# Optimization experiments

Measured on AMD Instinct MI355X. Metric: run time of the kernel, lower is better.

Reference implementation:

```python
import jax, jax.numpy as jnp
import numpy as np

S, C, E, G, H = 8192, 21, 128, 36, 1024  # seq_len, context_len, embed_dim, gazet_dim, hidden_dim
V_IN = 8000
T = 32              # tagset size incl. BOS/EOS
START, STOP = 30, 31
NEG = -10000.0


def setup_inputs() -> dict:
    key = jax.random.key(0)
    ks = jax.random.split(key, 10)
    contexts = jax.random.randint(ks[0], (S, C), 0, V_IN)
    gazet = jax.random.uniform(ks[1], (S, C, G), dtype=jnp.float32)
    train_labels = jax.random.randint(ks[2], (S,), 0, 30)  # base tags only
    emb = jax.random.normal(ks[3], (V_IN, E), dtype=jnp.float32) * 0.1
    D = C * (E + G)
    w1 = jax.random.normal(ks[4], (H, D), dtype=jnp.float32) / np.sqrt(D)
    b1 = jnp.zeros((H,), dtype=jnp.float32)
    w2 = jax.random.normal(ks[5], (T, H), dtype=jnp.float32) / np.sqrt(H)
    b2 = jnp.zeros((T,), dtype=jnp.float32)
    trans = jax.random.normal(ks[6], (T, T), dtype=jnp.float32)
    trans = trans.at[START, :].set(NEG)   # nothing transitions into START... (row = next tag)
    trans = trans.at[:, STOP].set(NEG)    # nothing leaves STOP (col = prev tag)
    return {"contexts": contexts, "gazet": gazet, "train_labels": train_labels,
            "emb": emb, "w1": w1, "b1": b1, "w2": w2, "b2": b2, "trans": trans}


def _feats(contexts, gazet, emb, w1, b1, w2, b2):
    x = jnp.concatenate([emb[contexts], gazet], axis=2)      # [S, C, E+G]
    x = x.reshape(x.shape[0], -1)                            # [S, C*(E+G)]
    h = jax.nn.relu(x @ w1.T + b1)                           # [S, H]  (dropout = identity in eval)
    return h @ w2.T + b2                                     # [S, T]


def _crf_forward(feats, trans):
    alpha0 = jnp.full((T,), NEG, dtype=feats.dtype).at[START].set(0.0)

    def step(alpha, feat):
        # scores[next, prev] = alpha[prev] + trans[next, prev] + feat[next]
        scores = alpha[None, :] + trans + feat[:, None]
        return jax.nn.logsumexp(scores, axis=1), None

    alpha, _ = jax.lax.scan(step, alpha0, feats)
    return jax.nn.logsumexp(alpha + trans[STOP])


def _gold_score(feats, tags, trans):
    tags_ext = jnp.concatenate([jnp.array([START], dtype=tags.dtype), tags])
    trans_sc = jnp.sum(trans[tags_ext[1:], tags_ext[:-1]])
    emit_sc = jnp.sum(feats[jnp.arange(feats.shape[0]), tags])
    return trans_sc + emit_sc + trans[STOP, tags[-1]]


def reference(contexts, gazet, train_labels, emb, w1, b1, w2, b2, trans):
    feats = _feats(contexts, gazet, emb, w1, b1, w2, b2)
    fwd = _crf_forward(feats, trans)
    gold = _gold_score(feats, train_labels, trans)
    return fwd - gold  # neg_log_likelihood (scalar)
```

## Files before the change

### kernel.cpp

```cpp
#include <hip/hip_runtime.h>

#define S_LEN 8192
#define C_CTX 21
#define E_DIM 128
#define G_DIM 36
#define H_DIM 1024
#define T_TAG 32
#define D_RAW 3444
#define DP 3456
#define GZP 768
#define START_TAG 30
#define STOP_TAG 31
#define NEGV -10000.0f
#define K_CHUNKS 64
#define L_CHUNK 128

typedef __bf16 bf16_t;
typedef __bf16 bf16x4 __attribute__((ext_vector_type(4)));
typedef __bf16 bf16x8 __attribute__((ext_vector_type(8)));
typedef float  f32x4  __attribute__((ext_vector_type(4)));

__device__ inline void async_copy16(const bf16_t* g, bf16_t* l) {
    __builtin_amdgcn_global_load_lds(
        (const __attribute__((address_space(1))) void*)g,
        (__attribute__((address_space(3))) void*)l, 16, 0, 0);
}

__global__ void build_all(const int* __restrict__ ctx, const float* __restrict__ gz,
                          const float* __restrict__ emb, const float* __restrict__ w1,
                          bf16_t* __restrict__ Xg, bf16_t* __restrict__ W,
                          bf16_t* __restrict__ EB) {
    const int b = blockIdx.x;
    if (b < 1024) {
        const int h = b;
        for (int g = threadIdx.x; g < DP / 4; g += 256) {
            bf16x4 o;
            if (g < 672) {
                const int knew = g * 4;
                const float4 v = *(const float4*)&w1[(size_t)h * D_RAW + (knew >> 7) * 164 + (knew & 127)];
                o = bf16x4{(bf16_t)v.x, (bf16_t)v.y, (bf16_t)v.z, (bf16_t)v.w};
            } else {
                const int m = g * 4 - 2688;
                float t[4];
#pragma unroll
                for (int u = 0; u < 4; ++u) {
                    const int mm = m + u;
                    t[u] = (mm < 756) ? w1[(size_t)h * D_RAW + (mm / 36) * 164 + 128 + (mm % 36)] : 0.f;
                }
                o = bf16x4{(bf16_t)t[0], (bf16_t)t[1], (bf16_t)t[2], (bf16_t)t[3]};
            }
            *(bf16x4*)&W[(size_t)h * DP + g * 4] = o;
        }
    } else if (b < 3072) {
        const int s_base = (b - 1024) * 4;
        for (int g = threadIdx.x; g < 4 * 192; g += 256) {
            const int r = g / 192, gg = g - r * 192;
            const int s = s_base + r;
            bf16x4 o = bf16x4{(bf16_t)0.f, (bf16_t)0.f, (bf16_t)0.f, (bf16_t)0.f};
            if (gg < 189) {
                const float4 v = *(const float4*)&gz[(size_t)s * 756 + gg * 4];
                o = bf16x4{(bf16_t)v.x, (bf16_t)v.y, (bf16_t)v.z, (bf16_t)v.w};
            }
            *(bf16x4*)&Xg[(size_t)s * GZP + gg * 4] = o;
        }
    } else {
        const size_t base = (size_t)(b - 3072) * 2048;
        for (int g = threadIdx.x; g < 512; g += 256) {
            const float4 v = *(const float4*)&emb[base + g * 4];
            bf16x4 o = bf16x4{(bf16_t)v.x, (bf16_t)v.y, (bf16_t)v.z, (bf16_t)v.w};
            *(bf16x4*)&EB[base + g * 4] = o;
        }
    }
}

__global__ __launch_bounds__(512) void gemm1(const int* __restrict__ ctx,
                                             const bf16_t* __restrict__ EB,
                                             const bf16_t* __restrict__ Xg,
                                             const bf16_t* __restrict__ W,
                                             const float* __restrict__ b1,
                                             const float* __restrict__ w2,
                                             const float* __restrict__ b2,
                                             float* __restrict__ Fp) {
    __shared__ bf16_t As[3][256 * 64];
    __shared__ bf16_t Bs[3][128 * 64];
    __shared__ unsigned short ctxs[256 * 21];
    const int tid  = threadIdx.x;
    const int wave = tid >> 6, lane = tid & 63;
    const int s0 = blockIdx.x * 256, h0 = blockIdx.y * 128;
    const int wm = (wave >> 1) * 64;
    const int wn = (wave & 1) * 64;

    const int arow = tid >> 3;
    const int akg  = (tid & 7) ^ (arow & 7);
    const bf16_t* gB = W + (size_t)(h0 + arow) * DP + akg * 8;

    const int lrow  = lane & 15;
    const int khalf = lane >> 4;
    const int lr7   = lrow & 7;

#define STAGE_B(buf, k0, i) async_copy16(gB + (size_t)(i) * 64 * DP + (k0), &Bs[buf][((i) * 512 + tid) * 8])

    for (int j = tid; j < 256 * C_CTX; j += 512)
        ctxs[j] = (unsigned short)ctx[s0 * C_CTX + j];
    asm volatile("s_waitcnt lgkmcnt(0)" ::: "memory");
    __builtin_amdgcn_s_barrier();

    {
        const int cva = ctxs[(arow      ) * 21], cvb = ctxs[(arow +  64) * 21];
        const int cvc = ctxs[(arow + 128) * 21], cvd = ctxs[(arow + 192) * 21];
        const int ea0 = akg * 8;
        async_copy16(EB + (size_t)cva * 128 + ea0, &As[0][(0 * 512 + tid) * 8]);
        async_copy16(EB + (size_t)cvb * 128 + ea0, &As[0][(1 * 512 + tid) * 8]);
        async_copy16(EB + (size_t)cvc * 128 + ea0, &As[0][(2 * 512 + tid) * 8]);
        async_copy16(EB + (size_t)cvd * 128 + ea0, &As[0][(3 * 512 + tid) * 8]);
        STAGE_B(0, 0, 0); STAGE_B(0, 0, 1);
        const int ea1 = 64 + akg * 8;
        async_copy16(EB + (size_t)cva * 128 + ea1, &As[1][(0 * 512 + tid) * 8]);
        async_copy16(EB + (size_t)cvb * 128 + ea1, &As[1][(1 * 512 + tid) * 8]);
        async_copy16(EB + (size_t)cvc * 128 + ea1, &As[1][(2 * 512 + tid) * 8]);
        async_copy16(EB + (size_t)cvd * 128 + ea1, &As[1][(3 * 512 + tid) * 8]);
        STAGE_B(1, 64, 0); STAGE_B(1, 64, 1);
    }
    asm volatile("s_waitcnt vmcnt(6)" ::: "memory");
    __builtin_amdgcn_s_barrier();

    f32x4 acc[4][4] = {};
    const int NT = DP / 64;
    int rb = 0;
    for (int t = 0; t < NT; ++t) {
        const int  sb = (rb == 0) ? 2 : rb - 1;
        const int  tt = t + 2;
        const bool st = tt < NT;
        const bool semb = st && (tt < 42);

        int cv0 = 0, cv1 = 0, cv2 = 0, cv3 = 0;
        if (semb) {
            const int c_ = tt >> 1;
            cv0 = ctxs[(arow      ) * 21 + c_];
            cv1 = ctxs[(arow +  64) * 21 + c_];
            cv2 = ctxs[(arow + 128) * 21 + c_];
            cv3 = ctxs[(arow + 192) * 21 + c_];
        }

        bf16x8 a[2][2][2];
        bf16x8 b[2][2][2];
#pragma unroll
        for (int ks = 0; ks < 2; ++ks) {
            const int kgr = ((ks * 4 + khalf) ^ lr7) * 8;
#pragma unroll
            for (int sp = 0; sp < 2; ++sp)
#pragma unroll
                for (int mt = 0; mt < 2; ++mt)
                    a[sp][ks][mt] = *(const bf16x8*)&As[rb][(wm + sp * 32 + mt * 16 + lrow) * 64 + kgr];
#pragma unroll
            for (int qn = 0; qn < 2; ++qn)
#pragma unroll
                for (int nt = 0; nt < 2; ++nt)
                    b[qn][ks][nt] = *(const bf16x8*)&Bs[rb][(wn + qn * 32 + nt * 16 + lrow) * 64 + kgr];
        }
        if (st) {
            if (semb) {
                const int e0 = (tt & 1) * 64 + akg * 8;
                async_copy16(EB + (size_t)cv0 * 128 + e0, &As[sb][(0 * 512 + tid) * 8]);
                async_copy16(EB + (size_t)cv1 * 128 + e0, &As[sb][(1 * 512 + tid) * 8]);
                async_copy16(EB + (size_t)cv2 * 128 + e0, &As[sb][(2 * 512 + tid) * 8]);
                async_copy16(EB + (size_t)cv3 * 128 + e0, &As[sb][(3 * 512 + tid) * 8]);
            } else {
                const int m0 = (tt - 42) * 64 + akg * 8;
#pragma unroll
                for (int i = 0; i < 4; ++i)
                    async_copy16(Xg + (size_t)(s0 + arow + i * 64) * GZP + m0, &As[sb][(i * 512 + tid) * 8]);
            }
            STAGE_B(sb, tt * 64, 0); STAGE_B(sb, tt * 64, 1);
        }
        __builtin_amdgcn_s_barrier();
        __builtin_amdgcn_s_setprio(1);
#pragma unroll
        for (int ks = 0; ks < 2; ++ks)
#pragma unroll
            for (int sp = 0; sp < 2; ++sp)
#pragma unroll
                for (int qn = 0; qn < 2; ++qn)
#pragma unroll
                    for (int mt = 0; mt < 2; ++mt)
#pragma unroll
                        for (int nt = 0; nt < 2; ++nt)
                            acc[sp * 2 + mt][qn * 2 + nt] = __builtin_amdgcn_mfma_f32_16x16x32_bf16(
                                a[sp][ks][mt], b[qn][ks][nt], acc[sp * 2 + mt][qn * 2 + nt], 0, 0, 0);
        __builtin_amdgcn_s_setprio(0);
        if (st)              asm volatile("s_waitcnt vmcnt(6)" ::: "memory");
        else if (t + 1 < NT) asm volatile("s_waitcnt vmcnt(0)" ::: "memory");
        __builtin_amdgcn_s_barrier();
        rb = (rb == 2) ? 0 : rb + 1;
    }
#undef STAGE_B

    bf16_t* Hl = &As[0][0];
    bf16_t* Wl = &Bs[0][0];

    {
        const int t8 = tid >> 4;
        const int hl = tid & 15;
        const float* wsrc = w2 + (size_t)t8 * H_DIM + h0 + hl * 8;
        const float4 y0 = *(const float4*)wsrc;
        const float4 y1 = *(const float4*)(wsrc + 4);
        bf16x8 wv = {(bf16_t)y0.x, (bf16_t)y0.y, (bf16_t)y0.z, (bf16_t)y0.w,
                     (bf16_t)y1.x, (bf16_t)y1.y, (bf16_t)y1.z, (bf16_t)y1.w};
        *(bf16x8*)&Wl[(t8 * 16 + (hl ^ (t8 & 7))) * 8] = wv;
    }

    const int crow = (lane >> 4) * 4;
    const int ccol = lane & 15;
#pragma unroll
    for (int nt = 0; nt < 4; ++nt) {
        const int jl = wn + nt * 16 + ccol;
        const float bv = b1[h0 + jl];
#pragma unroll
        for (int mt = 0; mt < 4; ++mt) {
#pragma unroll
            for (int r = 0; r < 4; ++r) {
                const int sl = wm + mt * 16 + crow + r;
                const float v = acc[mt][nt][r] + bv;
                Hl[sl * 128 + ((jl >> 3) ^ (sl & 7)) * 8 + (jl & 7)] = (bf16_t)fmaxf(v, 0.f);
            }
        }
    }
    __syncthreads();

    f32x4 acc2[2][2] = {};
    const int wm2 = wave * 32;
#pragma unroll
    for (int ks = 0; ks < 4; ++ks) {
        const int slot = ((ks * 4 + khalf) ^ lr7) * 8;
        bf16x8 ah[2], bw[2];
#pragma unroll
        for (int mt = 0; mt < 2; ++mt)
            ah[mt] = *(const bf16x8*)&Hl[(wm2 + mt * 16 + lrow) * 128 + slot];
#pragma unroll
        for (int nt = 0; nt < 2; ++nt)
            bw[nt] = *(const bf16x8*)&Wl[(nt * 16 + lrow) * 128 + slot];
#pragma unroll
        for (int mt = 0; mt < 2; ++mt)
#pragma unroll
            for (int nt = 0; nt < 2; ++nt)
                acc2[mt][nt] = __builtin_amdgcn_mfma_f32_16x16x32_bf16(ah[mt], bw[nt], acc2[mt][nt], 0, 0, 0);
    }
    const int bj = h0 >> 7;
#pragma unroll
    for (int nt = 0; nt < 2; ++nt) {
        const int tcol = nt * 16 + ccol;
        const float badd = (bj == 7) ? b2[tcol] : 0.f;
#pragma unroll
        for (int mt = 0; mt < 2; ++mt) {
#pragma unroll
            for (int r = 0; r < 4; ++r) {
                const int sr = s0 + wm2 + mt * 16 + crow + r;
                Fp[((size_t)bj * S_LEN + sr) * T_TAG + tcol] = acc2[mt][nt][r] + badd;
            }
        }
    }
}

__global__ __launch_bounds__(512) void crfA(const float* __restrict__ Fp,
                                            const float* __restrict__ trans,
                                            float* __restrict__ QT,
                                            float* __restrict__ sigma,
                                            float* __restrict__ Fsum) {
    __shared__ float fl[L_CHUNK * 32];
    __shared__ float vb[8][64];
    const int c    = blockIdx.x >> 2;
    const int tid  = threadIdx.x;
    const int wave = tid >> 6;
    const int lane = tid & 63;
    const int n    = lane & 31;
    const int h    = lane >> 5;
    const int p    = ((blockIdx.x & 3) << 3) + wave;
    const int s0   = c * L_CHUNK;
    for (int i = tid; i < L_CHUNK * 32; i += 512) {
        const size_t idx = (size_t)s0 * 32 + i;
        float accf = 0.f;
#pragma unroll
        for (int j = 0; j < 8; ++j) accf += Fp[(size_t)j * S_LEN * T_TAG + idx];
        fl[i] = accf;
        Fsum[idx] = accf;
    }
    __syncthreads();

    float etl[16];
#pragma unroll
    for (int j = 0; j < 16; ++j) etl[j] = __expf(trans[n * 32 + h * 16 + j]);

    float* vrow = &vb[wave][0];
    float v  = __expf(trans[n * 32 + p] + fl[n]);
    float sg = 0.f;
    for (int s = 1; s < L_CHUNK; ++s) {
        vrow[lane] = v;
        __builtin_amdgcn_s_waitcnt(0xC07F);
        float a0 = 0.f, a1 = 0.f, a2 = 0.f, a3 = 0.f;
#pragma unroll
        for (int q = 0; q < 4; ++q) {
            const float4 wv = *(const float4*)&vrow[h * 16 + q * 4];
            a0 = __builtin_fmaf(etl[q * 4 + 0], wv.x, a0);
            a1 = __builtin_fmaf(etl[q * 4 + 1], wv.y, a1);
            a2 = __builtin_fmaf(etl[q * 4 + 2], wv.z, a2);
            a3 = __builtin_fmaf(etl[q * 4 + 3], wv.w, a3);
        }
        float part = (a0 + a1) + (a2 + a3);
        part += __shfl_xor(part, 32);
        v = __expf(fl[s * 32 + n]) * part;
        if ((s & 7) == 7) {
            float m = v;
#pragma unroll
            for (int off = 16; off; off >>= 1) m = fmaxf(m, __shfl_xor(m, off, 32));
            if (m > 0.f) { v *= 1.0f / m; sg += __logf(m); }
        }
    }
    if (h == 0) {
        QT[(c * 32 + p) * 32 + n] = v;
        if (n == 0) sigma[c * 32 + p] = sg;
    }
}

__global__ __launch_bounds__(1024) void crf_fold(const float* __restrict__ Qin,
                                                 const float* __restrict__ Sin,
                                                 const int fold, const int final,
                                                 float* __restrict__ Qout,
                                                 float* __restrict__ Sout,
                                                 const float* __restrict__ trans,
                                                 const float* __restrict__ F,
                                                 const int* __restrict__ lab,
                                                 float* __restrict__ out) {
    __shared__ float A[32][33];
    __shared__ float M[32][33];
    __shared__ float sgf[32];
    __shared__ float gred[16];
    __shared__ float gold_s;

    const int t = threadIdx.x;
    const int p = t >> 5, n = t & 31;
    const int c0 = blockIdx.x * fold;

    if (final) {
        float ga = 0.f;
        for (int s = t; s < S_LEN; s += 1024) {
            const int tg = lab[s];
            ga += F[(size_t)s * T_TAG + tg];
            const int tp = (s == 0) ? START_TAG : lab[s - 1];
            ga += trans[tg * T_TAG + tp];
        }
        if (t == 0) ga += trans[STOP_TAG * T_TAG + lab[S_LEN - 1]];
#pragma unroll
        for (int off = 32; off; off >>= 1) ga += __shfl_down(ga, off, 64);
        if ((t & 63) == 0) gred[t >> 6] = ga;
    }

    A[n][p] = Qin[(size_t)(c0 * 32 + p) * 32 + n];
    float sA = Sin[c0 * 32 + p];
    float mreg = Qin[(size_t)((c0 + 1) * 32 + p) * 32 + n];

    for (int i = 1; i < fold; ++i) {
        const float sMn = Sin[(c0 + i) * 32 + n];
        float mmax = sMn;
#pragma unroll
        for (int off = 16; off; off >>= 1) mmax = fmaxf(mmax, __shfl_xor(mmax, off, 32));
        const float sMp = Sin[(c0 + i) * 32 + p];
        __syncthreads();
        M[n][p] = mreg * __expf(sMp - mmax);
        if (i + 1 < fold) mreg = Qin[(size_t)((c0 + i + 1) * 32 + p) * 32 + n];
        __syncthreads();
        float acc = 0.f;
#pragma unroll 8
        for (int k = 0; k < 32; ++k)
            acc += M[n][k] * A[k][p];
        float cm = acc;
#pragma unroll
        for (int off = 16; off; off >>= 1) cm = fmaxf(cm, __shfl_xor(cm, off, 32));
        cm = fmaxf(cm, 1e-37f);
        __syncthreads();
        A[n][p] = acc / cm;
        sA = sA + mmax + __logf(cm);
    }
    __syncthreads();

    if (!final) {
        Qout[(size_t)(blockIdx.x * 32 + p) * 32 + n] = A[n][p];
        if (n == 0) Sout[blockIdx.x * 32 + p] = sA;
        return;
    }

    if (n == 0) sgf[p] = sA;
    if (t == 0) {
        float s = 0.f;
#pragma unroll
        for (int i = 0; i < 16; ++i) s += gred[i];
        gold_s = s;
    }
    __syncthreads();
    if (t < 32) {
        float v = A[t][START_TAG] * __expf(trans[STOP_TAG * T_TAG + t]);
#pragma unroll
        for (int off = 16; off; off >>= 1) v += __shfl_xor(v, off, 32);
        if (t == 0) out[0] = sgf[START_TAG] + __logf(v) - gold_s;
    }
}

extern "C" void kernel_launch(void* const* d_in, const int* in_sizes, int n_in,
                              void* d_out, int out_size, void* d_ws, size_t ws_size,
                              hipStream_t stream) {
    const int*   ctx   = (const int*)d_in[0];
    const float* gz    = (const float*)d_in[1];
    const int*   lab   = (const int*)d_in[2];
    const float* emb   = (const float*)d_in[3];
    const float* w1    = (const float*)d_in[4];
    const float* b1    = (const float*)d_in[5];
    const float* w2    = (const float*)d_in[6];
    const float* b2    = (const float*)d_in[7];
    const float* trans = (const float*)d_in[8];
    float* out = (float*)d_out;

    char* ws = (char*)d_ws;
    bf16_t* W1b = (bf16_t*)(ws + 0);
    bf16_t* EB  = (bf16_t*)(ws + 7077888);
    bf16_t* Xg  = (bf16_t*)(ws + 9126400);
    float*  Fp  = (float*)(ws + 21709312);
    float*  F   = (float*)(ws + 30097920);
    float*  QT  = (float*)(ws + 31146496);
    float*  sg  = (float*)(ws + 31408640);
    float*  Q1  = (float*)(ws + 31416832);
    float*  S1  = (float*)(ws + 31449600);

    build_all<<<3572, 256, 0, stream>>>(ctx, gz, emb, w1, Xg, W1b, EB);
    gemm1<<<dim3(S_LEN / 256, H_DIM / 128), 512, 0, stream>>>(ctx, EB, Xg, W1b, b1, w2, b2, Fp);
    crfA<<<K_CHUNKS * 4, 512, 0, stream>>>(Fp, trans, QT, sg, F);
    crf_fold<<<8, 1024, 0, stream>>>(QT, sg, 8, 0, Q1, S1, trans, F, lab, out);
    crf_fold<<<1, 1024, 0, stream>>>(Q1, S1, 8, 1, nullptr, nullptr, trans, F, lab, out);
}
```

Baseline: 240.9 us.

## Shrink GEMM1 tile to 128x128 with 256 threads and double buffering

The fused GEMM1 kernel moves from 256x128 tiles with 512 threads and a 3-stage async pipeline to 128x128 tiles with 256 threads and a 2-stage buffer. Each iteration now waits for all outstanding loads (vmcnt(0)) before the barrier. This cuts LDS use per block and doubles the grid, aiming for more resident blocks and better CU coverage. In exchange, each loaded W1 tile is reused across fewer rows, global traffic rises, and less load latency is hidden behind compute. The epilogue loop for w2 staging is adjusted to fit the smaller thread count.

```diff
diff --git a/kernel.cpp b/kernel.cpp
--- a/kernel.cpp
+++ b/kernel.cpp
@@ -73,7 +73,7 @@
     }
 }
 
-__global__ __launch_bounds__(512) void gemm1(const int* __restrict__ ctx,
+__global__ __launch_bounds__(256) void gemm1(const int* __restrict__ ctx,
                                              const bf16_t* __restrict__ EB,
                                              const bf16_t* __restrict__ Xg,
                                              const bf16_t* __restrict__ W,
@@ -81,12 +81,12 @@
                                              const float* __restrict__ w2,
                                              const float* __restrict__ b2,
                                              float* __restrict__ Fp) {
-    __shared__ bf16_t As[3][256 * 64];
-    __shared__ bf16_t Bs[3][128 * 64];
-    __shared__ unsigned short ctxs[256 * 21];
+    __shared__ bf16_t As[2][128 * 64];
+    __shared__ bf16_t Bs[2][128 * 64];
+    __shared__ unsigned short ctxs[128 * 21];
     const int tid  = threadIdx.x;
     const int wave = tid >> 6, lane = tid & 63;
-    const int s0 = blockIdx.x * 256, h0 = blockIdx.y * 128;
+    const int s0 = blockIdx.x * 128, h0 = blockIdx.y * 128;
     const int wm = (wave >> 1) * 64;
     const int wn = (wave & 1) * 64;
 
@@ -98,49 +98,31 @@
     const int khalf = lane >> 4;
     const int lr7   = lrow & 7;
 
-#define STAGE_B(buf, k0, i) async_copy16(gB + (size_t)(i) * 64 * DP + (k0), &Bs[buf][((i) * 512 + tid) * 8])
-
-    for (int j = tid; j < 256 * C_CTX; j += 512)
+    for (int j = tid; j < 128 * C_CTX; j += 256)
         ctxs[j] = (unsigned short)ctx[s0 * C_CTX + j];
     asm volatile("s_waitcnt lgkmcnt(0)" ::: "memory");
     __builtin_amdgcn_s_barrier();
 
     {
-        const int cva = ctxs[(arow      ) * 21], cvb = ctxs[(arow +  64) * 21];
-        const int cvc = ctxs[(arow + 128) * 21], cvd = ctxs[(arow + 192) * 21];
-        const int ea0 = akg * 8;
-        async_copy16(EB + (size_t)cva * 128 + ea0, &As[0][(0 * 512 + tid) * 8]);
-        async_copy16(EB + (size_t)cvb * 128 + ea0, &As[0][(1 * 512 + tid) * 8]);
-        async_copy16(EB + (size_t)cvc * 128 + ea0, &As[0][(2 * 512 + tid) * 8]);
-        async_copy16(EB + (size_t)cvd * 128 + ea0, &As[0][(3 * 512 + tid) * 8]);
-        STAGE_B(0, 0, 0); STAGE_B(0, 0, 1);
-        const int ea1 = 64 + akg * 8;
-        async_copy16(EB + (size_t)cva * 128 + ea1, &As[1][(0 * 512 + tid) * 8]);
-        async_copy16(EB + (size_t)cvb * 128 + ea1, &As[1][(1 * 512 + tid) * 8]);
-        async_copy16(EB + (size_t)cvc * 128 + ea1, &As[1][(2 * 512 + tid) * 8]);
-        async_copy16(EB + (size_t)cvd * 128 + ea1, &As[1][(3 * 512 + tid) * 8]);
-        STAGE_B(1, 64, 0); STAGE_B(1, 64, 1);
-    }
-    asm volatile("s_waitcnt vmcnt(6)" ::: "memory");
+        const int e0 = akg * 8;
+#pragma unroll
+        for (int i = 0; i < 4; ++i) {
+            const int cv = ctxs[(i * 32 + arow) * 21];
+            async_copy16(EB + (size_t)cv * 128 + e0, &As[0][(i * 256 + tid) * 8]);
+        }
+#pragma unroll
+        for (int i = 0; i < 4; ++i)
+            async_copy16(gB + (size_t)i * 32 * DP, &Bs[0][(i * 256 + tid) * 8]);
+    }
+    asm volatile("s_waitcnt vmcnt(0)" ::: "memory");
     __builtin_amdgcn_s_barrier();
 
     f32x4 acc[4][4] = {};
     const int NT = DP / 64;
-    int rb = 0;
     for (int t = 0; t < NT; ++t) {
-        const int  sb = (rb == 0) ? 2 : rb - 1;
-        const int  tt = t + 2;
+        const int cur = t & 1, nxt = cur ^ 1;
+        const int tt = t + 1;
         const bool st = tt < NT;
-        const bool semb = st && (tt < 42);
-
-        int cv0 = 0, cv1 = 0, cv2 = 0, cv3 = 0;
-        if (semb) {
-            const int c_ = tt >> 1;
-            cv0 = ctxs[(arow      ) * 21 + c_];
-            cv1 = ctxs[(arow +  64) * 21 + c_];
-            cv2 = ctxs[(arow + 128) * 21 + c_];
-            cv3 = ctxs[(arow + 192) * 21 + c_];
-        }
 
         bf16x8 a[2][2][2];
         bf16x8 b[2][2][2];
@@ -151,29 +133,32 @@
             for (int sp = 0; sp < 2; ++sp)
 #pragma unroll
                 for (int mt = 0; mt < 2; ++mt)
-                    a[sp][ks][mt] = *(const bf16x8*)&As[rb][(wm + sp * 32 + mt * 16 + lrow) * 64 + kgr];
+                    a[sp][ks][mt] = *(const bf16x8*)&As[cur][(wm + sp * 32 + mt * 16 + lrow) * 64 + kgr];
 #pragma unroll
             for (int qn = 0; qn < 2; ++qn)
 #pragma unroll
                 for (int nt = 0; nt < 2; ++nt)
-                    b[qn][ks][nt] = *(const bf16x8*)&Bs[rb][(wn + qn * 32 + nt * 16 + lrow) * 64 + kgr];
+                    b[qn][ks][nt] = *(const bf16x8*)&Bs[cur][(wn + qn * 32 + nt * 16 + lrow) * 64 + kgr];
         }
         if (st) {
-            if (semb) {
+            if (tt < 42) {
+                const int c_ = tt >> 1;
                 const int e0 = (tt & 1) * 64 + akg * 8;
-                async_copy16(EB + (size_t)cv0 * 128 + e0, &As[sb][(0 * 512 + tid) * 8]);
-                async_copy16(EB + (size_t)cv1 * 128 + e0, &As[sb][(1 * 512 + tid) * 8]);
-                async_copy16(EB + (size_t)cv2 * 128 + e0, &As[sb][(2 * 512 + tid) * 8]);
-                async_copy16(EB + (size_t)cv3 * 128 + e0, &As[sb][(3 * 512 + tid) * 8]);
+#pragma unroll
+                for (int i = 0; i < 4; ++i) {
+                    const int cv = ctxs[(i * 32 + arow) * 21 + c_];
+                    async_copy16(EB + (size_t)cv * 128 + e0, &As[nxt][(i * 256 + tid) * 8]);
+                }
             } else {
                 const int m0 = (tt - 42) * 64 + akg * 8;
 #pragma unroll
                 for (int i = 0; i < 4; ++i)
-                    async_copy16(Xg + (size_t)(s0 + arow + i * 64) * GZP + m0, &As[sb][(i * 512 + tid) * 8]);
+                    async_copy16(Xg + (size_t)(s0 + i * 32 + arow) * GZP + m0, &As[nxt][(i * 256 + tid) * 8]);
             }
-            STAGE_B(sb, tt * 64, 0); STAGE_B(sb, tt * 64, 1);
-        }
-        __builtin_amdgcn_s_barrier();
+#pragma unroll
+            for (int i = 0; i < 4; ++i)
+                async_copy16(gB + (size_t)i * 32 * DP + tt * 64, &Bs[nxt][(i * 256 + tid) * 8]);
+        }
         __builtin_amdgcn_s_setprio(1);
 #pragma unroll
         for (int ks = 0; ks < 2; ++ks)
@@ -188,19 +173,17 @@
                             acc[sp * 2 + mt][qn * 2 + nt] = __builtin_amdgcn_mfma_f32_16x16x32_bf16(
                                 a[sp][ks][mt], b[qn][ks][nt], acc[sp * 2 + mt][qn * 2 + nt], 0, 0, 0);
         __builtin_amdgcn_s_setprio(0);
-        if (st)              asm volatile("s_waitcnt vmcnt(6)" ::: "memory");
-        else if (t + 1 < NT) asm volatile("s_waitcnt vmcnt(0)" ::: "memory");
+        if (st) asm volatile("s_waitcnt vmcnt(0)" ::: "memory");
         __builtin_amdgcn_s_barrier();
-        rb = (rb == 2) ? 0 : rb + 1;
-    }
-#undef STAGE_B
+    }
 
     bf16_t* Hl = &As[0][0];
     bf16_t* Wl = &Bs[0][0];
 
-    {
-        const int t8 = tid >> 4;
-        const int hl = tid & 15;
+#pragma unroll
+    for (int rep = 0; rep < 2; ++rep) {
+        const int t8 = tid >> 3;
+        const int hl = (tid & 7) * 2 + rep;
         const float* wsrc = w2 + (size_t)t8 * H_DIM + h0 + hl * 8;
         const float4 y0 = *(const float4*)wsrc;
         const float4 y1 = *(const float4*)(wsrc + 4);
@@ -430,7 +413,7 @@
     float*  S1  = (float*)(ws + 31449600);
 
     build_all<<<3572, 256, 0, stream>>>(ctx, gz, emb, w1, Xg, W1b, EB);
-    gemm1<<<dim3(S_LEN / 256, H_DIM / 128), 512, 0, stream>>>(ctx, EB, Xg, W1b, b1, w2, b2, Fp);
+    gemm1<<<dim3(S_LEN / 128, H_DIM / 128), 256, 0, stream>>>(ctx, EB, Xg, W1b, b1, w2, b2, Fp);
     crfA<<<K_CHUNKS * 4, 512, 0, stream>>>(Fp, trans, QT, sg, F);
     crf_fold<<<8, 1024, 0, stream>>>(QT, sg, 8, 0, Q1, S1, trans, F, lab, out);
     crf_fold<<<1, 1024, 0, stream>>>(Q1, S1, 8, 1, nullptr, nullptr, trans, F, lab, out);
```

New measurement: 230.1 us. -4.5%, faster.
